# Kernel optimization log

Hardware: AMD Instinct MI355X
Metric: run time of the kernel (lower is better)

## Reference

```python
import jax, jax.numpy as jnp
import numpy as np

NUM_CLASSES = 100
EPS = 1e-8  # torch F.cosine_similarity default eps


def setup_inputs() -> dict:
    key = jax.random.key(0)
    k1, k2 = jax.random.split(key)
    feat = jax.random.normal(k1, (100000, 512), dtype=jnp.float32)
    label = jax.random.randint(k2, (100000,), 0, NUM_CLASSES, dtype=jnp.int64)
    return {"feat": feat, "label": label}


def reference(feat, label):
    # Per-class mean (segment mean) -- replaces the Python loop over classes.
    sums = jax.ops.segment_sum(feat, label, num_segments=NUM_CLASSES)          # [C, D]
    counts = jax.ops.segment_sum(jnp.ones_like(label, dtype=feat.dtype), label,
                                 num_segments=NUM_CLASSES)                      # [C]
    means = sums / jnp.maximum(counts, 1.0)[:, None]                            # [C, D]

    # Only the gathered (own-class) column of the sim matrix is returned,
    # so compute cos(feat[i], means[label[i]]) directly.
    cent = means[label]                                                         # [N, D]
    dot = jnp.sum(feat * cent, axis=-1)                                         # [N]
    n_feat = jnp.maximum(jnp.linalg.norm(feat, axis=-1), EPS)
    n_cent = jnp.maximum(jnp.linalg.norm(cent, axis=-1), EPS)
    return dot / (n_feat * n_cent)
```

## Files before the change

kernel.cpp:

```cpp
#include <hip/hip_runtime.h>
#include <hip/hip_bf16.h>

#define NCLS 100
#define DIM  512
#define EPSV 1e-8f
#define NSPLIT 16
#define IDXBUF 512
#define SCAT_ROWS 1024

__global__ __launch_bounds__(256) void hist_kernel(const int* __restrict__ label,
                                                   int* __restrict__ cnt, int n) {
    __shared__ int h[NCLS];
    for (int i = threadIdx.x; i < NCLS; i += 256) h[i] = 0;
    __syncthreads();
    for (int i = blockIdx.x * 256 + threadIdx.x; i < n; i += gridDim.x * 256)
        atomicAdd(&h[label[i]], 1);
    __syncthreads();
    for (int i = threadIdx.x; i < NCLS; i += 256) {
        int v = h[i];
        if (v) atomicAdd(&cnt[i], v);
    }
}

__global__ __launch_bounds__(128) void scan_kernel(const int* __restrict__ cnt,
                                                   int* __restrict__ base,
                                                   int* __restrict__ cursor) {
    __shared__ int a[128];
    const int t = threadIdx.x;
    a[t] = (t < NCLS) ? cnt[t] : 0;
    __syncthreads();
    #pragma unroll
    for (int off = 1; off < 128; off <<= 1) {
        int v = (t >= off) ? a[t - off] : 0;
        __syncthreads();
        a[t] += v;
        __syncthreads();
    }
    if (t < NCLS) {
        int excl = a[t] - cnt[t];
        base[t] = excl;
        cursor[t] = excl;
    }
}

__global__ __launch_bounds__(256) void scatter_kernel(const int* __restrict__ label,
                                                      int* __restrict__ cursor,
                                                      int* __restrict__ perm, int n) {
    __shared__ int h[NCLS];
    __shared__ int starts[NCLS];
    const int tid = threadIdx.x;
    for (int i = tid; i < NCLS; i += 256) h[i] = 0;
    __syncthreads();

    const int r0 = blockIdx.x * SCAT_ROWS;
    int c[4], lr[4];
    #pragma unroll
    for (int k = 0; k < 4; ++k) {
        const int r = r0 + k * 256 + tid;
        if (r < n) { c[k] = label[r]; lr[k] = atomicAdd(&h[c[k]], 1); }
        else c[k] = -1;
    }
    __syncthreads();
    for (int i = tid; i < NCLS; i += 256)
        starts[i] = h[i] ? atomicAdd(&cursor[i], h[i]) : 0;
    __syncthreads();
    #pragma unroll
    for (int k = 0; k < 4; ++k)
        if (c[k] >= 0) perm[starts[c[k]] + lr[k]] = r0 + k * 256 + tid;
}

__global__ __launch_bounds__(256) void segsum_kernel(const float* __restrict__ feat,
                                                     const int* __restrict__ perm,
                                                     const int* __restrict__ base,
                                                     const int* __restrict__ cnt,
                                                     float* __restrict__ sums) {
    const int s = blockIdx.x;
    const int c = blockIdx.y;
    const int m = cnt[c];
    const int b = base[c];
    const int jlo = b + (m * s) / NSPLIT;
    const int jhi = b + (m * (s + 1)) / NSPLIT;

    __shared__ int idx[IDXBUF];
    const int tid  = threadIdx.x;
    const int half = tid >> 7;
    const int dq   = (tid & 127) * 4;

    float4 acc = {0.0f, 0.0f, 0.0f, 0.0f};

    for (int j0 = jlo; j0 < jhi; j0 += IDXBUF) {
        const int batch = min(IDXBUF, jhi - j0);
        __syncthreads();
        for (int i = tid; i < batch; i += 256) idx[i] = perm[j0 + i];
        __syncthreads();
        int i = half;
        for (; i + 14 < batch; i += 16) {
            float4 v[8];
            #pragma unroll
            for (int u = 0; u < 8; ++u)
                v[u] = *(const float4*)(feat + (size_t)idx[i + 2 * u] * DIM + dq);
            #pragma unroll
            for (int u = 0; u < 8; ++u) {
                acc.x += v[u].x; acc.y += v[u].y; acc.z += v[u].z; acc.w += v[u].w;
            }
        }
        for (; i < batch; i += 2) {
            float4 v = *(const float4*)(feat + (size_t)idx[i] * DIM + dq);
            acc.x += v.x; acc.y += v.y; acc.z += v.z; acc.w += v.w;
        }
    }
    if (m > 0) {
        float* dst = &sums[(size_t)c * DIM + dq];
        atomicAdd(dst + 0, acc.x); atomicAdd(dst + 1, acc.y);
        atomicAdd(dst + 2, acc.z); atomicAdd(dst + 3, acc.w);
    }
}

__global__ __launch_bounds__(256) void finalize_kernel(const float* __restrict__ sums,
                                                       const int* __restrict__ cnt,
                                                       float* __restrict__ mhat) {
    const int c = blockIdx.x;
    const float inv = 1.0f / fmaxf((float)cnt[c], 1.0f);
    const int t = threadIdx.x;
    float m0 = sums[(size_t)c * DIM + t] * inv;
    float m1 = sums[(size_t)c * DIM + 256 + t] * inv;
    float ss = m0 * m0 + m1 * m1;
    #pragma unroll
    for (int off = 32; off; off >>= 1) ss += __shfl_down(ss, off, 64);
    __shared__ float red[4];
    if ((t & 63) == 0) red[t >> 6] = ss;
    __syncthreads();
    const float tot = red[0] + red[1] + red[2] + red[3];
    const float q = 1.0f / fmaxf(sqrtf(tot), EPSV);
    mhat[(size_t)c * DIM + t] = m0 * q;
    mhat[(size_t)c * DIM + 256 + t] = m1 * q;
}

__global__ __launch_bounds__(256) void cos_kernel(const float* __restrict__ feat,
                                                  const int* __restrict__ label,
                                                  const float* __restrict__ mhat,
                                                  float* __restrict__ out, int n) {
    const int lane = threadIdx.x & 63;
    const int wv   = threadIdx.x >> 6;
    const int cl   = lane >> 4;
    const int t    = lane & 15;

    const int row = blockIdx.x * 16 + wv * 4 + cl;
    const bool ok = row < n;
    const int rr = ok ? row : (n - 1);

    const int c = label[rr];
    const float4* f4 = (const float4*)(feat + (size_t)rr * DIM);
    const float4* m4 = (const float4*)(mhat + (size_t)c  * DIM);

    float4 a[8], b[8];
    #pragma unroll
    for (int j = 0; j < 8; ++j) a[j] = f4[t + 16 * j];
    #pragma unroll
    for (int j = 0; j < 8; ++j) b[j] = m4[t + 16 * j];

    float dot = 0.0f, nf = 0.0f;
    #pragma unroll
    for (int j = 0; j < 8; ++j) {
        dot += a[j].x * b[j].x + a[j].y * b[j].y + a[j].z * b[j].z + a[j].w * b[j].w;
        nf  += a[j].x * a[j].x + a[j].y * a[j].y + a[j].z * a[j].z + a[j].w * a[j].w;
    }

    #pragma unroll
    for (int off = 8; off; off >>= 1) {
        dot += __shfl_xor(dot, off, 64);
        nf  += __shfl_xor(nf,  off, 64);
    }
    if (t == 0 && ok) {
        out[row] = dot / fmaxf(sqrtf(nf), EPSV);
    }
}

extern "C" void kernel_launch(void* const* d_in, const int* in_sizes, int n_in,
                              void* d_out, int out_size, void* d_ws, size_t ws_size,
                              hipStream_t stream) {
    const float* feat  = (const float*)d_in[0];
    const int*   label = (const int*)d_in[1];
    float*       out   = (float*)d_out;
    const int n = in_sizes[0] / DIM;

    float* sums   = (float*)d_ws;
    int*   cnt    = (int*)(sums + NCLS * DIM);
    float* mhat   = (float*)(cnt + 128);
    int*   base   = (int*)(mhat + NCLS * DIM);
    int*   cursor = base + 128;
    int*   perm   = cursor + 128;

    hipMemsetAsync(d_ws, 0, (NCLS * DIM + 128) * sizeof(float), stream);

    hist_kernel<<<160, 256, 0, stream>>>(label, cnt, n);
    scan_kernel<<<1, 128, 0, stream>>>(cnt, base, cursor);
    scatter_kernel<<<(n + SCAT_ROWS - 1) / SCAT_ROWS, 256, 0, stream>>>(label, cursor, perm, n);

    dim3 sg(NSPLIT, NCLS);
    segsum_kernel<<<sg, 256, 0, stream>>>(feat, perm, base, cnt, sums);

    finalize_kernel<<<NCLS, 256, 0, stream>>>(sums, cnt, mhat);

    cos_kernel<<<(n + 15) / 16, 256, 0, stream>>>(feat, label, mhat, out, n);
}
```

Baseline: 331.4 us.

## Replace sort-based segment sum with streaming LDS-atomic per-chunk partial sums

Drops the histogram/scan/scatter permutation pipeline and the gathered segment-sum. Each block now streams a contiguous row chunk and one 128-wide slice of features, accumulating per-class sums in shared memory with swizzled LDS atomics. It writes per-chunk partials that the finalize kernel reduces. This removes the random gather, three kernel launches and the perm traffic. In exchange it relies on LDS float atomics, uses a 51KB shared buffer that lowers occupancy, and writes 128 partial copies for finalize to reduce.

After: 516.3 us. 55.8% more time.

```diff
diff --git a/kernel.cpp b/kernel.cpp
--- a/kernel.cpp
+++ b/kernel.cpp
@@ -1,130 +1,108 @@
 #include <hip/hip_runtime.h>
-#include <hip/hip_bf16.h>
 
 #define NCLS 100
 #define DIM  512
 #define EPSV 1e-8f
-#define NSPLIT 16
-#define IDXBUF 512
-#define SCAT_ROWS 1024
 
-__global__ __launch_bounds__(256) void hist_kernel(const int* __restrict__ label,
-                                                   int* __restrict__ cnt, int n) {
-    __shared__ int h[NCLS];
-    for (int i = threadIdx.x; i < NCLS; i += 256) h[i] = 0;
+#define CHUNKS  128
+#define SLICES  4
+#define SLICE_D 128
+#define LBATCH  800
+
+__global__ __launch_bounds__(256) void sum_kernel(const float* __restrict__ feat,
+                                                  const int* __restrict__ label,
+                                                  float* __restrict__ partial,
+                                                  int* __restrict__ cnt, int n) {
+    __shared__ float acc[NCLS * SLICE_D];
+    __shared__ int   lab[LBATCH];
+    __shared__ int   hcnt[NCLS];
+
+    const int tid = threadIdx.x;
+    const int s   = blockIdx.x;
+    const int ch  = blockIdx.y;
+
+    for (int i = tid; i < NCLS * SLICE_D; i += 256) acc[i] = 0.0f;
+    if (s == 0)
+        for (int i = tid; i < NCLS; i += 256) hcnt[i] = 0;
+
+    const int rpc  = (n + CHUNKS - 1) / CHUNKS;
+    const int r0   = ch * rpc;
+    const int rows = min(rpc, n - r0);
+    const int g    = tid >> 5;
+    const int l    = tid & 31;
+    const int swz  = (l >> 3) & 3;
+    const float* fbase = feat + (size_t)s * SLICE_D + (size_t)l * 4;
+
+    for (int b0 = 0; b0 < rows; b0 += LBATCH) {
+        const int bn = min(LBATCH, rows - b0);
+        __syncthreads();
+        for (int i = tid; i < bn; i += 256) lab[i] = label[r0 + b0 + i];
+        __syncthreads();
+
+        int i = g;
+        for (; i + 24 < bn; i += 32) {
+            float4 v[4]; int c[4];
+            #pragma unroll
+            for (int u = 0; u < 4; ++u) {
+                const int r = r0 + b0 + i + 8 * u;
+                c[u] = lab[i + 8 * u];
+                v[u] = *(const float4*)(fbase + (size_t)r * DIM);
+            }
+            #pragma unroll
+            for (int u = 0; u < 4; ++u) {
+                float* a = &acc[c[u] * SLICE_D + l * 4];
+                atomicAdd(&a[0 ^ swz], v[u].x);
+                atomicAdd(&a[1 ^ swz], v[u].y);
+                atomicAdd(&a[2 ^ swz], v[u].z);
+                atomicAdd(&a[3 ^ swz], v[u].w);
+                if (s == 0 && l == 0) atomicAdd(&hcnt[c[u]], 1);
+            }
+        }
+        for (; i < bn; i += 8) {
+            const int c = lab[i];
+            float4 v = *(const float4*)(fbase + (size_t)(r0 + b0 + i) * DIM);
+            float* a = &acc[c * SLICE_D + l * 4];
+            atomicAdd(&a[0 ^ swz], v.x);
+            atomicAdd(&a[1 ^ swz], v.y);
+            atomicAdd(&a[2 ^ swz], v.z);
+            atomicAdd(&a[3 ^ swz], v.w);
+            if (s == 0 && l == 0) atomicAdd(&hcnt[c], 1);
+        }
+    }
     __syncthreads();
-    for (int i = blockIdx.x * 256 + threadIdx.x; i < n; i += gridDim.x * 256)
-        atomicAdd(&h[label[i]], 1);
-    __syncthreads();
-    for (int i = threadIdx.x; i < NCLS; i += 256) {
-        int v = h[i];
-        if (v) atomicAdd(&cnt[i], v);
-    }
+
+    float* dst = partial + ((size_t)ch * SLICES + s) * (NCLS * SLICE_D);
+    for (int i = tid; i < NCLS * SLICE_D; i += 256) dst[i] = acc[i];
+    if (s == 0)
+        for (int i = tid; i < NCLS; i += 256)
+            if (hcnt[i]) atomicAdd(&cnt[i], hcnt[i]);
 }
 
-__global__ __launch_bounds__(128) void scan_kernel(const int* __restrict__ cnt,
-                                                   int* __restrict__ base,
-                                                   int* __restrict__ cursor) {
-    __shared__ int a[128];
-    const int t = threadIdx.x;
-    a[t] = (t < NCLS) ? cnt[t] : 0;
-    __syncthreads();
-    #pragma unroll
-    for (int off = 1; off < 128; off <<= 1) {
-        int v = (t >= off) ? a[t - off] : 0;
-        __syncthreads();
-        a[t] += v;
-        __syncthreads();
-    }
-    if (t < NCLS) {
-        int excl = a[t] - cnt[t];
-        base[t] = excl;
-        cursor[t] = excl;
-    }
-}
-
-__global__ __launch_bounds__(256) void scatter_kernel(const int* __restrict__ label,
-                                                      int* __restrict__ cursor,
-                                                      int* __restrict__ perm, int n) {
-    __shared__ int h[NCLS];
-    __shared__ int starts[NCLS];
-    const int tid = threadIdx.x;
-    for (int i = tid; i < NCLS; i += 256) h[i] = 0;
-    __syncthreads();
-
-    const int r0 = blockIdx.x * SCAT_ROWS;
-    int c[4], lr[4];
-    #pragma unroll
-    for (int k = 0; k < 4; ++k) {
-        const int r = r0 + k * 256 + tid;
-        if (r < n) { c[k] = label[r]; lr[k] = atomicAdd(&h[c[k]], 1); }
-        else c[k] = -1;
-    }
-    __syncthreads();
-    for (int i = tid; i < NCLS; i += 256)
-        starts[i] = h[i] ? atomicAdd(&cursor[i], h[i]) : 0;
-    __syncthreads();
-    #pragma unroll
-    for (int k = 0; k < 4; ++k)
-        if (c[k] >= 0) perm[starts[c[k]] + lr[k]] = r0 + k * 256 + tid;
-}
-
-__global__ __launch_bounds__(256) void segsum_kernel(const float* __restrict__ feat,
-                                                     const int* __restrict__ perm,
-                                                     const int* __restrict__ base,
-                                                     const int* __restrict__ cnt,
-                                                     float* __restrict__ sums) {
-    const int s = blockIdx.x;
-    const int c = blockIdx.y;
-    const int m = cnt[c];
-    const int b = base[c];
-    const int jlo = b + (m * s) / NSPLIT;
-    const int jhi = b + (m * (s + 1)) / NSPLIT;
-
-    __shared__ int idx[IDXBUF];
-    const int tid  = threadIdx.x;
-    const int half = tid >> 7;
-    const int dq   = (tid & 127) * 4;
-
-    float4 acc = {0.0f, 0.0f, 0.0f, 0.0f};
-
-    for (int j0 = jlo; j0 < jhi; j0 += IDXBUF) {
-        const int batch = min(IDXBUF, jhi - j0);
-        __syncthreads();
-        for (int i = tid; i < batch; i += 256) idx[i] = perm[j0 + i];
-        __syncthreads();
-        int i = half;
-        for (; i + 14 < batch; i += 16) {
-            float4 v[8];
-            #pragma unroll
-            for (int u = 0; u < 8; ++u)
-                v[u] = *(const float4*)(feat + (size_t)idx[i + 2 * u] * DIM + dq);
-            #pragma unroll
-            for (int u = 0; u < 8; ++u) {
-                acc.x += v[u].x; acc.y += v[u].y; acc.z += v[u].z; acc.w += v[u].w;
-            }
-        }
-        for (; i < batch; i += 2) {
-            float4 v = *(const float4*)(feat + (size_t)idx[i] * DIM + dq);
-            acc.x += v.x; acc.y += v.y; acc.z += v.z; acc.w += v.w;
-        }
-    }
-    if (m > 0) {
-        float* dst = &sums[(size_t)c * DIM + dq];
-        atomicAdd(dst + 0, acc.x); atomicAdd(dst + 1, acc.y);
-        atomicAdd(dst + 2, acc.z); atomicAdd(dst + 3, acc.w);
-    }
-}
-
-__global__ __launch_bounds__(256) void finalize_kernel(const float* __restrict__ sums,
+__global__ __launch_bounds__(256) void finalize_kernel(const float* __restrict__ partial,
                                                        const int* __restrict__ cnt,
                                                        float* __restrict__ mhat) {
     const int c = blockIdx.x;
+    const int t = threadIdx.x;
     const float inv = 1.0f / fmaxf((float)cnt[c], 1.0f);
-    const int t = threadIdx.x;
-    float m0 = sums[(size_t)c * DIM + t] * inv;
-    float m1 = sums[(size_t)c * DIM + 256 + t] * inv;
-    float ss = m0 * m0 + m1 * m1;
+
+    float m[2];
+    #pragma unroll
+    for (int h = 0; h < 2; ++h) {
+        const int d    = t + 256 * h;
+        const int sl   = d >> 7;
+        const int d7   = d & 127;
+        const int lsub = d7 >> 2;
+        const int slot = (d7 & ~3) | ((d & 3) ^ ((lsub >> 3) & 3));
+        const float* p = partial + (size_t)sl * (NCLS * SLICE_D)
+                                 + (size_t)c * SLICE_D + slot;
+        float a = 0.0f;
+        #pragma unroll 4
+        for (int ch = 0; ch < CHUNKS; ++ch)
+            a += p[(size_t)ch * (SLICES * NCLS * SLICE_D)];
+        m[h] = a * inv;
+    }
+
+    float ss = m[0] * m[0] + m[1] * m[1];
     #pragma unroll
     for (int off = 32; off; off >>= 1) ss += __shfl_down(ss, off, 64);
     __shared__ float red[4];
@@ -132,8 +110,8 @@
     __syncthreads();
     const float tot = red[0] + red[1] + red[2] + red[3];
     const float q = 1.0f / fmaxf(sqrtf(tot), EPSV);
-    mhat[(size_t)c * DIM + t] = m0 * q;
-    mhat[(size_t)c * DIM + 256 + t] = m1 * q;
+    mhat[(size_t)c * DIM + t]       = m[0] * q;
+    mhat[(size_t)c * DIM + 256 + t] = m[1] * q;
 }
 
 __global__ __launch_bounds__(256) void cos_kernel(const float* __restrict__ feat,
@@ -184,23 +162,14 @@
     float*       out   = (float*)d_out;
     const int n = in_sizes[0] / DIM;
 
-    float* sums   = (float*)d_ws;
-    int*   cnt    = (int*)(sums + NCLS * DIM);
-    float* mhat   = (float*)(cnt + 128);
-    int*   base   = (int*)(mhat + NCLS * DIM);
-    int*   cursor = base + 128;
-    int*   perm   = cursor + 128;
+    int*   cnt     = (int*)d_ws;
+    float* mhat    = (float*)(cnt + 128);
+    float* partial = mhat + NCLS * DIM;
 
-    hipMemsetAsync(d_ws, 0, (NCLS * DIM + 128) * sizeof(float), stream);
+    hipMemsetAsync(cnt, 0, 128 * sizeof(int), stream);
 
-    hist_kernel<<<160, 256, 0, stream>>>(label, cnt, n);
-    scan_kernel<<<1, 128, 0, stream>>>(cnt, base, cursor);
-    scatter_kernel<<<(n + SCAT_ROWS - 1) / SCAT_ROWS, 256, 0, stream>>>(label, cursor, perm, n);
-
-    dim3 sg(NSPLIT, NCLS);
-    segsum_kernel<<<sg, 256, 0, stream>>>(feat, perm, base, cnt, sums);
-
-    finalize_kernel<<<NCLS, 256, 0, stream>>>(sums, cnt, mhat);
-
+    dim3 sg(SLICES, CHUNKS);
+    sum_kernel<<<sg, 256, 0, stream>>>(feat, label, partial, cnt, n);
+    finalize_kernel<<<NCLS, 256, 0, stream>>>(partial, cnt, mhat);
     cos_kernel<<<(n + 15) / 16, 256, 0, stream>>>(feat, label, mhat, out, n);
 }
```
